# Optimization experiments

Hardware: AMD Instinct MI355X
Metric: run time of the kernel (lower is better)

Reference implementation:

```python
import jax, jax.numpy as jnp
import numpy as np

EPS = 1e-6
NEG = -10000.0

def compute_alibi_slopes(n_head):
    # standard ALiBi slopes for power-of-two head counts: 2^{-8(i+1)/n}
    start = 2.0 ** (-8.0 / n_head)
    return jnp.asarray([start ** (i + 1) for i in range(n_head)], dtype=jnp.float32)

def setup_inputs() -> dict:
    key = jax.random.key(0)
    k1, k2, k3 = jax.random.split(key, 3)
    B, T, C, H = 2, 2048, 1024, 16
    x = jax.random.normal(k1, (B, T, C), dtype=jnp.float32)
    # torch nn.Linear weights are [out_features, in_features]
    w_qkv = jax.random.normal(k2, (3 * C, C), dtype=jnp.float32) * (C ** -0.5)
    w_out = jax.random.normal(k3, (C, C), dtype=jnp.float32) * (C ** -0.5)
    alibi_slopes = compute_alibi_slopes(H)
    return {"x": x, "w_qkv": w_qkv, "w_out": w_out, "alibi_slopes": alibi_slopes}

def rational_softmax(scores, eps=EPS):
    # algebraic sigmoid 0.5*(1 + x/sqrt(1+x^2)) normalized along last axis
    num = 0.5 * (1.0 + scores * jax.lax.rsqrt(1.0 + scores * scores))
    return num / (jnp.sum(num, axis=-1, keepdims=True) + eps)

def reference(x, w_qkv, w_out, alibi_slopes):
    B, T, C = x.shape
    H = alibi_slopes.shape[0]
    D = C // H
    scale = 1.0 / jnp.sqrt(jnp.float32(D))
    qkv = (x @ w_qkv.T).reshape(B, T, 3, H, D)
    qkv = jnp.transpose(qkv, (2, 0, 3, 1, 4))  # [3,B,H,T,D]
    q, k, v = qkv[0], qkv[1], qkv[2]
    scores = jnp.einsum("bhtd,bhsd->bhts", q, k) * scale  # [B,H,T,T]
    pos = jnp.arange(T)
    rel = pos[:, None] - pos[None, :]  # [T,T]
    alibi = -jnp.abs(rel).astype(jnp.float32) * alibi_slopes[None, :, None, None]
    scores = scores + alibi
    causal = rel < 0  # strictly upper triangle (j > i)
    scores = jnp.where(causal[None, None], NEG, scores)
    probs = rational_softmax(scores, EPS)
    out = jnp.einsum("bhts,bhsd->bhtd", probs, v)  # [B,H,T,D]
    out = jnp.transpose(out, (0, 2, 1, 3)).reshape(B, T, C)
    return out @ w_out.T
```

## Files before the change

### kernel.cpp

```cpp
#include <hip/hip_runtime.h>
#include <stdint.h>

typedef __attribute__((ext_vector_type(8))) short bf16x8;
typedef __attribute__((ext_vector_type(4))) float f32x4;
typedef __attribute__((ext_vector_type(16))) float f32x16;

#define MFMA_16x16x32(a, b, c) __builtin_amdgcn_mfma_f32_16x16x32_bf16((a), (b), (c), 0, 0, 0)
#define MFMA_32x32x16(a, b, c) __builtin_amdgcn_mfma_f32_32x32x16_bf16((a), (b), (c), 0, 0, 0)

__device__ __forceinline__ short f2bf(float f) {
  union { float f; uint32_t u; } x;
  x.f = f;
  uint32_t r = x.u + 0x7fffu + ((x.u >> 16) & 1u);
  return (short)(r >> 16);
}

__device__ __forceinline__ uint32_t cvt_pk_bf16(float lo, float hi) {
  uint32_t r;
  asm("v_cvt_pk_bf16_f32 %0, %1, %2" : "=v"(r) : "v"(lo), "v"(hi));
  return r;
}

__device__ __forceinline__ void gload_lds16(const short* g, short* l) {
  __builtin_amdgcn_global_load_lds(
      (const __attribute__((address_space(1))) void*)g,
      (__attribute__((address_space(3))) void*)l, 16, 0, 0);
}

__global__ __launch_bounds__(256) void cast_all(const float* __restrict__ x,
                                                const float* __restrict__ wq,
                                                const float* __restrict__ wo,
                                                short* __restrict__ xb,
                                                short* __restrict__ wqb,
                                                short* __restrict__ wob) {
  int i = blockIdx.x * 256 + threadIdx.x;
  const float* s;
  short* d;
  int off;
  float sc = 1.0f;
  if (i < 524288) { s = x; d = xb; off = i; }
  else if (i < 917504) {
    s = wq; d = wqb; off = i - 524288;
    if (off < 131072) sc = 0.125f;
  }
  else { s = wo; d = wob; off = i - 917504; }
  const float4* sp = (const float4*)s;
  float4 v0 = sp[(size_t)off * 2 + 0];
  float4 v1 = sp[(size_t)off * 2 + 1];
  bf16x8 o;
  o[0] = f2bf(v0.x * sc); o[1] = f2bf(v0.y * sc); o[2] = f2bf(v0.z * sc); o[3] = f2bf(v0.w * sc);
  o[4] = f2bf(v1.x * sc); o[5] = f2bf(v1.y * sc); o[6] = f2bf(v1.z * sc); o[7] = f2bf(v1.w * sc);
  *(bf16x8*)(d + (size_t)off * 8) = o;
}

template <int OUT_BF16>
__global__ __launch_bounds__(512, 2) void gemm256(const short* __restrict__ A,
                                                  const short* __restrict__ B,
                                                  void* __restrict__ Cp,
                                                  int M, int N, int K, int ntN) {
  __shared__ short Al[2][2][128 * 64];
  __shared__ short Bl[2][2][128 * 64];

  const int tid = threadIdx.x;
  const int wv = tid >> 6, lane = tid & 63;
  const int wr = wv >> 2, wc = wv & 3;
  const int lrow = lane & 15, kgrp = lane >> 4;
  const int l3 = lrow & 7;
  const int ck0 = ((kgrp ^ l3)) * 8;
  const int ck1 = ((kgrp ^ l3) ^ 4) * 8;

  const int nwg = gridDim.x;
  const int orig = blockIdx.x;
  const int wg = (orig & 7) * (nwg >> 3) + (orig >> 3);
  const int by = wg / ntN, bx = wg % ntN;
  const int row0 = by * 256, col0 = bx * 256;

  const int r_ = tid >> 3;
  const int cs_ = ((tid & 7) ^ (r_ & 7)) * 8;

  const int NT = K >> 6;
  const int NI = NT >> 1;
  const int NTm1 = NT - 1;

  auto stgA = [&](int slot, int h, int j, int kt) {
    gload_lds16(A + (size_t)(row0 + h * 128 + j * 64 + r_) * K + kt * 64 + cs_,
                &Al[slot][h][j * 4096 + wv * 512]);
  };
  auto stgB = [&](int slot, int h, int j, int kt) {
    gload_lds16(B + (size_t)(col0 + h * 128 + j * 64 + r_) * K + kt * 64 + cs_,
                &Bl[slot][h][j * 4096 + wv * 512]);
  };

  f32x4 acc[8][4] = {};

  const int boff = ((wc & 1) * 64 + lrow) * 64;
  const int bh = wc >> 1;

  stgB(0, 0, 0, 0); stgB(0, 0, 1, 0); stgB(0, 1, 0, 0); stgB(0, 1, 1, 0);
  stgA(0, 0, 0, 0); stgA(0, 0, 1, 0); stgA(0, 1, 0, 0); stgA(0, 1, 1, 0);
  stgB(1, 0, 0, 1); stgB(1, 0, 1, 1); stgB(1, 1, 0, 1); stgB(1, 1, 1, 1);
  asm volatile("s_waitcnt vmcnt(4)" ::: "memory");
  __builtin_amdgcn_s_barrier();

  for (int i = 0; i < NI; ++i) {
    const int ktB1 = (2 * i + 1);
    const int ktP2 = (2 * i + 2 > NTm1) ? NTm1 : 2 * i + 2;
    const int ktP3 = (2 * i + 3 > NTm1) ? NTm1 : 2 * i + 3;
#pragma unroll
    for (int s = 0; s < 2; ++s) {
      bf16x8 bfr[4][2];
#pragma unroll
      for (int q = 0; q < 4; ++q) {
        if (q == 0) {
#pragma unroll
          for (int n = 0; n < 4; ++n) {
            bfr[n][0] = *(const bf16x8*)(&Bl[s][bh][boff + n * 1024 + ck0]);
            bfr[n][1] = *(const bf16x8*)(&Bl[s][bh][boff + n * 1024 + ck1]);
          }
        }
        bf16x8 afr[2][2];
#pragma unroll
        for (int mm = 0; mm < 2; ++mm) {
          const int m = q * 2 + mm;
          afr[mm][0] = *(const bf16x8*)(&Al[s][wr][lrow * 64 + m * 1024 + ck0]);
          afr[mm][1] = *(const bf16x8*)(&Al[s][wr][lrow * 64 + m * 1024 + ck1]);
        }
        if (s == 0) {
          if (q == 0) { stgA(1, 0, 0, ktB1); stgA(1, 0, 1, ktB1); stgA(1, 1, 0, ktB1); stgA(1, 1, 1, ktB1); }
          else if (q == 1) { stgB(0, 0, 0, ktP2); stgB(0, 0, 1, ktP2); }
          else if (q == 2) { stgB(0, 1, 0, ktP2); stgB(0, 1, 1, ktP2); }
        } else {
          if (q == 0) { stgA(0, 0, 0, ktP2); stgA(0, 0, 1, ktP2); stgA(0, 1, 0, ktP2); stgA(0, 1, 1, ktP2); }
          else if (q == 1) { stgB(1, 0, 0, ktP3); stgB(1, 0, 1, ktP3); }
          else if (q == 2) { stgB(1, 1, 0, ktP3); stgB(1, 1, 1, ktP3); }
        }
        __builtin_amdgcn_sched_barrier(0);
        __builtin_amdgcn_s_barrier();
        asm volatile("s_waitcnt lgkmcnt(0)" ::: "memory");
        __builtin_amdgcn_sched_barrier(0);
        __builtin_amdgcn_s_setprio(1);
#pragma unroll
        for (int mm = 0; mm < 2; ++mm)
#pragma unroll
          for (int n = 0; n < 4; ++n)
#pragma unroll
            for (int kk = 0; kk < 2; ++kk)
              acc[q * 2 + mm][n] = MFMA_16x16x32(afr[mm][kk], bfr[n][kk], acc[q * 2 + mm][n]);
        __builtin_amdgcn_s_setprio(0);
        __builtin_amdgcn_sched_barrier(0);
        if (q == 3) {
          asm volatile("s_waitcnt vmcnt(4)" ::: "memory");
        }
        __builtin_amdgcn_s_barrier();
      }
    }
  }

  asm volatile("s_waitcnt vmcnt(0)" ::: "memory");

#pragma unroll
  for (int m = 0; m < 8; ++m) {
    const int grow = row0 + wr * 128 + m * 16 + kgrp * 4;
#pragma unroll
    for (int n = 0; n < 4; ++n) {
      const int gcol = col0 + wc * 64 + n * 16 + lrow;
#pragma unroll
      for (int j = 0; j < 4; ++j) {
        const size_t off = (size_t)(grow + j) * N + gcol;
        if (OUT_BF16) ((short*)Cp)[off] = f2bf(acc[m][n][j]);
        else          ((float*)Cp)[off] = acc[m][n][j];
      }
    }
  }
}

template <int OUT_BF16>
__global__ __launch_bounds__(256, 4) void gemm_bt64(const short* __restrict__ A,
                                                    const short* __restrict__ B,
                                                    void* __restrict__ Cp,
                                                    int M, int N, int K) {
  __shared__ short As[2][64 * 64];
  __shared__ short Bs[2][128 * 64];
  const int tid = threadIdx.x;
  const int wave = tid >> 6, lane = tid & 63;
  const int wr = wave >> 1, wc = wave & 1;
  const int row0 = blockIdx.y * 64, col0 = blockIdx.x * 128;
  const int lrow = lane & 15;
  const int kgrp = lane >> 4;
  const int l3 = lrow & 7;

  const int r_ = tid >> 3;
  const int cs_ = ((tid & 7) ^ (r_ & 7)) * 8;

  const int NT = K >> 6;

  auto STG = [&](int buf, int kt) {
#pragma unroll
    for (int it = 0; it < 2; ++it)
      gload_lds16(A + (size_t)(row0 + it * 32 + r_) * K + kt * 64 + cs_,
                  &As[buf][(it * 256 + wave * 64) * 8]);
#pragma unroll
    for (int it = 0; it < 4; ++it)
      gload_lds16(B + (size_t)(col0 + it * 32 + r_) * K + kt * 64 + cs_,
                  &Bs[buf][(it * 256 + wave * 64) * 8]);
  };

  f32x4 acc[2][4] = {};

  STG(0, 0);

  for (int kt = 0; kt < NT; ++kt) {
    __builtin_amdgcn_s_barrier();
    __builtin_amdgcn_sched_barrier(0);
    const int ktn = (kt + 1 >= NT) ? NT - 1 : kt + 1;
    STG((kt + 1) & 1, ktn);
    asm volatile("s_waitcnt vmcnt(6)" ::: "memory");
    __builtin_amdgcn_sched_barrier(0);
    const short* Ab = As[kt & 1];
    const short* Bb = Bs[kt & 1];
#pragma unroll
    for (int kk = 0; kk < 2; ++kk) {
      const int ck = ((kk * 4 + kgrp) ^ l3) * 8;
      bf16x8 a[2], b[4];
#pragma unroll
      for (int m = 0; m < 2; ++m)
        a[m] = *(const bf16x8*)(Ab + (wr * 32 + m * 16 + lrow) * 64 + ck);
#pragma unroll
      for (int n = 0; n < 4; ++n)
        b[n] = *(const bf16x8*)(Bb + (wc * 64 + n * 16 + lrow) * 64 + ck);
#pragma unroll
      for (int m = 0; m < 2; ++m)
#pragma unroll
        for (int n = 0; n < 4; ++n)
          acc[m][n] = MFMA_16x16x32(a[m], b[n], acc[m][n]);
    }
  }

  asm volatile("s_waitcnt vmcnt(0)" ::: "memory");

#pragma unroll
  for (int m = 0; m < 2; ++m) {
    int rbase = row0 + wr * 32 + m * 16 + kgrp * 4;
#pragma unroll
    for (int n = 0; n < 4; ++n) {
      int col = col0 + wc * 64 + n * 16 + lrow;
#pragma unroll
      for (int j = 0; j < 4; ++j) {
        size_t off = (size_t)(rbase + j) * N + col;
        if (OUT_BF16) ((short*)Cp)[off] = f2bf(acc[m][n][j]);
        else          ((float*)Cp)[off] = acc[m][n][j];
      }
    }
  }
}

__global__ __launch_bounds__(256) void transpose_v(const short* __restrict__ qkv,
                                                   short* __restrict__ vt) {
  const int T = 2048;
  __shared__ short sm[64][72];
  const int bh = blockIdx.y, h = bh & 15, b = bh >> 4;
  const int t0 = blockIdx.x * 64;
  const int tid = threadIdx.x;
#pragma unroll
  for (int p = 0; p < 2; ++p) {
    int idx = p * 256 + tid;
    int tl = idx >> 3, d0 = (idx & 7) * 8;
    bf16x8 v = *(const bf16x8*)(qkv + (b * T + t0 + tl) * 3072 + 2048 + h * 64 + d0);
    *(bf16x8*)(&sm[tl][d0]) = v;
  }
  __syncthreads();
#pragma unroll
  for (int p = 0; p < 2; ++p) {
    int idx = p * 256 + tid;
    int d = idx >> 3, ts0 = (idx & 7) * 8;
    bf16x8 o;
#pragma unroll
    for (int j = 0; j < 8; ++j) o[j] = sm[ts0 + j][d];
    *(bf16x8*)(vt + (bh * 64 + d) * T + t0 + ts0) = o;
  }
}

template <bool DIAG>
__device__ __forceinline__ void attn_sub(
    const short* __restrict__ Kb, const short* __restrict__ Vb,
    const bf16x8 (&qf)[4], const f32x16& crun,
    f32x16& acc0, f32x16& acc1, float (&den4)[4],
    int l31, int hi, int shalf, int mbits) {
  const int krow = l31 >> 1;
  const int kc0 = (l31 & 1) * 8 + hi;
  const int ss = shalf;
  __builtin_amdgcn_s_setprio(1);
  const bf16x8 kf0 = *(const bf16x8*)(Kb + (ss * 16 + krow) * 128 + (kc0 ^ krow) * 8);
  f32x16 s = MFMA_32x32x16(kf0, qf[0], crun);
#pragma unroll
  for (int kkd = 1; kkd < 4; ++kkd) {
    const bf16x8 kf = *(const bf16x8*)(Kb + (ss * 16 + krow) * 128 +
                                       ((kc0 + kkd * 2) ^ krow) * 8);
    s = MFMA_32x32x16(kf, qf[kkd], s);
  }
  __builtin_amdgcn_s_setprio(0);
  float nm[16];
#pragma unroll
  for (int v = 0; v < 16; ++v) {
    float x = s[v];
    if (DIAG) x = ((mbits >> v) & 1) ? -10000.0f : x;
    float t = fmaf(x, x, 1.0f);
    float num = fmaf(x * __builtin_amdgcn_rsqf(t), 0.5f, 0.5f);
    den4[v & 3] += num;
    nm[v] = num;
  }
#pragma unroll
  for (int k1 = 0; k1 < 2; ++k1) {
    union { uint32_t u[4]; bf16x8 v8; } pu;
#pragma unroll
    for (int w01 = 0; w01 < 2; ++w01) {
      uint32_t c0 = cvt_pk_bf16(nm[2 * w01 + 8 * k1], nm[2 * w01 + 8 * k1 + 1]);
      uint32_t c1 = cvt_pk_bf16(nm[2 * w01 + 8 * k1 + 4], nm[2 * w01 + 8 * k1 + 5]);
      asm volatile("v_permlane32_swap_b32 %0, %1" : "+v"(c0), "+v"(c1));
      pu.u[w01] = c0;
      pu.u[w01 + 2] = c1;
    }
    const int vsw = ((((l31 & 1) * 8) + ss * 4 + k1 * 2 + hi) ^ krow) * 8;
    const bf16x8 vf0 = *(const bf16x8*)(Vb + krow * 128 + vsw);
    const bf16x8 vf1 = *(const bf16x8*)(Vb + (16 + krow) * 128 + vsw);
    __builtin_amdgcn_s_setprio(1);
    acc0 = MFMA_32x32x16(pu.v8, vf0, acc0);
    acc1 = MFMA_32x32x16(pu.v8, vf1, acc1);
    __builtin_amdgcn_s_setprio(0);
  }
}

__device__ __constant__ int HPAIR[8][2] = {
  {15, 0}, {14, 1}, {13, 2}, {12, 3}, {11, 4}, {10, 5}, {9, 6}, {8, 7}};

__global__ __launch_bounds__(256, 3) void attn_kernel(const short* __restrict__ qkv,
                                                      const short* __restrict__ vt,
                                                      const float* __restrict__ slopes,
                                                      short* __restrict__ attn_out) {
  const int T = 2048, C = 1024, C3 = 3072;
  __shared__ short Kl[3][4096];
  __shared__ short Vl[3][4096];
  __shared__ float denm[64];

  const int tid = threadIdx.x, wv = tid >> 6, lane = tid & 63;
  const int l31 = lane & 31, hi = lane >> 5;
  const int wg = blockIdx.x;
  const int xcd = wg & 7, j = wg >> 3;
  const int bhsel = j & 3;
  const int qi = 31 - (j >> 2);
  const int h = HPAIR[xcd][bhsel & 1];
  const int b = bhsel >> 1;
  const int bh = b * 16 + h;
  const int qsub = wv >> 1, shalf = wv & 1;
  const float slope = slopes[h];
  const float s64 = slope * 64.0f;

  const int W = (int)(45.0f / (64.0f * slope)) + 2;
  const int kt0 = (qi - W > 0) ? (qi - W) : 0;

  int mbits = 0;
#pragma unroll
  for (int v = 0; v < 16; ++v) {
    int s32 = (v & 3) + 8 * (v >> 2) + 4 * hi;
    if (s32 > l31) mbits |= (1 << v);
  }
  int koff[2], voff[2];
#pragma unroll
  for (int p = 0; p < 2; ++p) {
    int idx = p * 256 + tid;
    int rho = idx >> 4, u = idx & 15, c = u ^ (rho & 15);
    koff[p] = (2 * rho + (c >> 3)) * C3 + (c & 7) * 8;
    voff[p] = (2 * rho + (c >> 3)) * T + (c & 7) * 8;
  }
  const short* kbase = qkv + (size_t)b * T * C3 + C + h * 64;
  const short* vbase = vt + (size_t)bh * 64 * T;

  auto STAGE = [&](int bufi, int kt) {
#pragma unroll
    for (int p = 0; p < 2; ++p)
      gload_lds16(kbase + (size_t)kt * 64 * C3 + koff[p], &Kl[bufi][(p * 256 + wv * 64) * 8]);
#pragma unroll
    for (int p = 0; p < 2; ++p)
      gload_lds16(vbase + kt * 64 + voff[p], &Vl[bufi][(p * 256 + wv * 64) * 8]);
  };

  const int qg = qi * 64 + qsub * 32 + l31;
  bf16x8 qf[4];
#pragma unroll
  for (int ks = 0; ks < 4; ++ks)
    qf[ks] = *(const bf16x8*)(qkv + (size_t)(b * T + qg) * C3 + h * 64 + ks * 16 + hi * 8);
  __builtin_amdgcn_sched_barrier(0);

  STAGE(0, kt0);
  STAGE(1, (kt0 + 1 > qi) ? qi : kt0 + 1);

  f32x16 crun;
#pragma unroll
  for (int v = 0; v < 16; ++v) {
    int s32 = (v & 3) + 8 * (v >> 2) + 4 * hi;
    crun[v] = slope * (float)(s32 - l31 + 32 * (shalf - qsub) + 64 * (kt0 - qi));
  }

  f32x16 acc0 = {}, acc1 = {};
  float den4[4] = {0.f, 0.f, 0.f, 0.f};

  int cA = 0;
  for (int kt = kt0; kt < qi; ++kt) {
    asm volatile("s_waitcnt vmcnt(4)" ::: "memory");
    __builtin_amdgcn_s_barrier();
    __builtin_amdgcn_sched_barrier(0);
    int cS = cA + 2; if (cS >= 3) cS -= 3;
    STAGE(cS, (kt + 2 > qi) ? qi : kt + 2);
    attn_sub<false>(Kl[cA], Vl[cA], qf, crun, acc0, acc1, den4, l31, hi, shalf, mbits);
#pragma unroll
    for (int v = 0; v < 16; ++v) crun[v] += s64;
    cA = (cA == 2) ? 0 : cA + 1;
  }
  asm volatile("s_waitcnt vmcnt(4)" ::: "memory");
  __builtin_amdgcn_s_barrier();
  if (!(qsub == 0 && shalf == 1)) {
    if (qsub == 1 && shalf == 0)
      attn_sub<false>(Kl[cA], Vl[cA], qf, crun, acc0, acc1, den4, l31, hi, shalf, mbits);
    else
      attn_sub<true>(Kl[cA], Vl[cA], qf, crun, acc0, acc1, den4, l31, hi, shalf, mbits);
  }
  __syncthreads();

  int sc = cA + 1; if (sc >= 3) sc -= 3;
  float den = (den4[0] + den4[1]) + (den4[2] + den4[3]);
  den += __shfl_xor(den, 32);

  if (shalf == 1) {
    float* mp = (float*)(qsub == 0 ? &Kl[sc][0] : &Vl[sc][0]);
#pragma unroll
    for (int i = 0; i < 16; ++i) {
      mp[i * 64 + lane] = acc0[i];
      mp[(16 + i) * 64 + lane] = acc1[i];
    }
    if (hi == 0) denm[qsub * 32 + l31] = den;
  }
  __syncthreads();

  if (shalf == 0) {
    const float* mp = (const float*)(qsub == 0 ? &Kl[sc][0] : &Vl[sc][0]);
    den += denm[qsub * 32 + l31];
#pragma unroll
    for (int i = 0; i < 16; ++i) {
      acc0[i] += mp[i * 64 + lane];
      acc1[i] += mp[(16 + i) * 64 + lane];
    }
    short* obase = attn_out + (size_t)(b * T + qi * 64 + qsub * 32) * C + h * 64;
#pragma unroll
    for (int v = 0; v < 16; ++v) {
      int ql = (v & 3) + 8 * (v >> 2) + 4 * hi;
      float dv = __int_as_float(__builtin_amdgcn_ds_bpermute(ql << 2, __float_as_int(den)));
      float r = __builtin_amdgcn_rcpf(dv + 1e-6f);
      obase[(size_t)ql * C + l31] = f2bf(acc0[v] * r);
      obase[(size_t)ql * C + 32 + l31] = f2bf(acc1[v] * r);
    }
  }
}

extern "C" void kernel_launch(void* const* d_in, const int* in_sizes, int n_in,
                              void* d_out, int out_size, void* d_ws, size_t ws_size,
                              hipStream_t stream) {
  const float* x      = (const float*)d_in[0];
  const float* w_qkv  = (const float*)d_in[1];
  const float* w_out  = (const float*)d_in[2];
  const float* slopes = (const float*)d_in[3];

  const int B = 2, T = 2048, C = 1024;
  const int M = B * T;
  const int N1 = 3 * C;

  char* ws = (char*)d_ws;
  short* x_bf    = (short*)(ws);
  short* wqkv_bf = (short*)(ws + 8388608);
  short* wout_bf = (short*)(ws + 14680064);
  short* qkv_bf  = (short*)(ws + 16777216);
  short* vt_bf   = (short*)(ws + 41943040);
  short* ao_bf   = (short*)(ws + 50331648);

  cast_all<<<4096, 256, 0, stream>>>(x, w_qkv, w_out, x_bf, wqkv_bf, wout_bf);

  gemm256<1><<<dim3((M / 256) * (N1 / 256)), 512, 0, stream>>>(x_bf, wqkv_bf, qkv_bf,
                                                               M, N1, C, N1 / 256);

  transpose_v<<<dim3(T / 64, 32), 256, 0, stream>>>(qkv_bf, vt_bf);

  attn_kernel<<<1024, 256, 0, stream>>>(qkv_bf, vt_bf, slopes, ao_bf);

  gemm_bt64<0><<<dim3(C / 128, M / 64), 256, 0, stream>>>(ao_bf, wout_bf, (float*)d_out, M, C, C);
}
```

Before: 102.3 us.

## Widen attention workgroups to 128 query rows sharing staged K/V tiles

The attention kernel now launches 512 workgroups of 512 threads, each covering a 128-row query block with four query groups that share the same triple-buffered K/V tiles in LDS. Each thread issues a single LDS-direct load per tile instead of two, and per-wave causal logic decides whether a tile is a full, diagonal-masked, or skipped block. This halves redundant K/V global loads across query blocks. In exchange, the waves above the diagonal idle on the last tile, the ALiBi window is widened to the larger block, and fewer, larger workgroups may reduce scheduling flexibility and load balance.

```diff
diff --git a/kernel.cpp b/kernel.cpp
--- a/kernel.cpp
+++ b/kernel.cpp
@@ -333,30 +333,33 @@
 __device__ __constant__ int HPAIR[8][2] = {
   {15, 0}, {14, 1}, {13, 2}, {12, 3}, {11, 4}, {10, 5}, {9, 6}, {8, 7}};
 
-__global__ __launch_bounds__(256, 3) void attn_kernel(const short* __restrict__ qkv,
+__global__ __launch_bounds__(512, 4) void attn_kernel(const short* __restrict__ qkv,
                                                       const short* __restrict__ vt,
                                                       const float* __restrict__ slopes,
                                                       short* __restrict__ attn_out) {
   const int T = 2048, C = 1024, C3 = 3072;
   __shared__ short Kl[3][4096];
   __shared__ short Vl[3][4096];
-  __shared__ float denm[64];
+  __shared__ float denm[128];
 
   const int tid = threadIdx.x, wv = tid >> 6, lane = tid & 63;
   const int l31 = lane & 31, hi = lane >> 5;
   const int wg = blockIdx.x;
   const int xcd = wg & 7, j = wg >> 3;
   const int bhsel = j & 3;
-  const int qi = 31 - (j >> 2);
+  const int qibase = 15 - (j >> 2);
   const int h = HPAIR[xcd][bhsel & 1];
   const int b = bhsel >> 1;
   const int bh = b * 16 + h;
-  const int qsub = wv >> 1, shalf = wv & 1;
+  const int g = wv >> 1, shalf = wv & 1;
   const float slope = slopes[h];
   const float s64 = slope * 64.0f;
 
+  const int qr0 = qibase * 128;
+  const int qi_hi = 2 * qibase + 1;
   const int W = (int)(45.0f / (64.0f * slope)) + 2;
-  const int kt0 = (qi - W > 0) ? (qi - W) : 0;
+  int kt0 = 2 * qibase - W; if (kt0 < 0) kt0 = 0;
+  const int myq = 4 * qibase + g;
 
   int mbits = 0;
 #pragma unroll
@@ -364,27 +367,18 @@
     int s32 = (v & 3) + 8 * (v >> 2) + 4 * hi;
     if (s32 > l31) mbits |= (1 << v);
   }
-  int koff[2], voff[2];
-#pragma unroll
-  for (int p = 0; p < 2; ++p) {
-    int idx = p * 256 + tid;
-    int rho = idx >> 4, u = idx & 15, c = u ^ (rho & 15);
-    koff[p] = (2 * rho + (c >> 3)) * C3 + (c & 7) * 8;
-    voff[p] = (2 * rho + (c >> 3)) * T + (c & 7) * 8;
-  }
+  const int rho = tid >> 4, u_ = tid & 15, c_ = u_ ^ (rho & 15);
+  const int koff = (2 * rho + (c_ >> 3)) * C3 + (c_ & 7) * 8;
+  const int voff = (2 * rho + (c_ >> 3)) * T + (c_ & 7) * 8;
   const short* kbase = qkv + (size_t)b * T * C3 + C + h * 64;
   const short* vbase = vt + (size_t)bh * 64 * T;
 
   auto STAGE = [&](int bufi, int kt) {
-#pragma unroll
-    for (int p = 0; p < 2; ++p)
-      gload_lds16(kbase + (size_t)kt * 64 * C3 + koff[p], &Kl[bufi][(p * 256 + wv * 64) * 8]);
-#pragma unroll
-    for (int p = 0; p < 2; ++p)
-      gload_lds16(vbase + kt * 64 + voff[p], &Vl[bufi][(p * 256 + wv * 64) * 8]);
+    gload_lds16(kbase + (size_t)kt * 64 * C3 + koff, &Kl[bufi][wv * 512]);
+    gload_lds16(vbase + kt * 64 + voff, &Vl[bufi][wv * 512]);
   };
 
-  const int qg = qi * 64 + qsub * 32 + l31;
+  const int qg = qr0 + g * 32 + l31;
   bf16x8 qf[4];
 #pragma unroll
   for (int ks = 0; ks < 4; ++ks)
@@ -392,64 +386,58 @@
   __builtin_amdgcn_sched_barrier(0);
 
   STAGE(0, kt0);
-  STAGE(1, (kt0 + 1 > qi) ? qi : kt0 + 1);
+  STAGE(1, (kt0 + 1 > qi_hi) ? qi_hi : kt0 + 1);
 
   f32x16 crun;
 #pragma unroll
   for (int v = 0; v < 16; ++v) {
     int s32 = (v & 3) + 8 * (v >> 2) + 4 * hi;
-    crun[v] = slope * (float)(s32 - l31 + 32 * (shalf - qsub) + 64 * (kt0 - qi));
+    crun[v] = slope * (float)(kt0 * 64 + shalf * 32 + s32 - qg);
   }
 
   f32x16 acc0 = {}, acc1 = {};
   float den4[4] = {0.f, 0.f, 0.f, 0.f};
 
   int cA = 0;
-  for (int kt = kt0; kt < qi; ++kt) {
+  for (int kt = kt0; kt <= qi_hi; ++kt) {
     asm volatile("s_waitcnt vmcnt(4)" ::: "memory");
     __builtin_amdgcn_s_barrier();
     __builtin_amdgcn_sched_barrier(0);
     int cS = cA + 2; if (cS >= 3) cS -= 3;
-    STAGE(cS, (kt + 2 > qi) ? qi : kt + 2);
-    attn_sub<false>(Kl[cA], Vl[cA], qf, crun, acc0, acc1, den4, l31, hi, shalf, mbits);
+    STAGE(cS, (kt + 2 > qi_hi) ? qi_hi : kt + 2);
+    const int drel = (2 * kt + shalf) - myq;
+    if (drel < 0)
+      attn_sub<false>(Kl[cA], Vl[cA], qf, crun, acc0, acc1, den4, l31, hi, shalf, mbits);
+    else if (drel == 0)
+      attn_sub<true>(Kl[cA], Vl[cA], qf, crun, acc0, acc1, den4, l31, hi, shalf, mbits);
 #pragma unroll
     for (int v = 0; v < 16; ++v) crun[v] += s64;
     cA = (cA == 2) ? 0 : cA + 1;
   }
-  asm volatile("s_waitcnt vmcnt(4)" ::: "memory");
-  __builtin_amdgcn_s_barrier();
-  if (!(qsub == 0 && shalf == 1)) {
-    if (qsub == 1 && shalf == 0)
-      attn_sub<false>(Kl[cA], Vl[cA], qf, crun, acc0, acc1, den4, l31, hi, shalf, mbits);
-    else
-      attn_sub<true>(Kl[cA], Vl[cA], qf, crun, acc0, acc1, den4, l31, hi, shalf, mbits);
-  }
   __syncthreads();
 
-  int sc = cA + 1; if (sc >= 3) sc -= 3;
   float den = (den4[0] + den4[1]) + (den4[2] + den4[3]);
   den += __shfl_xor(den, 32);
 
+  float* mp = (g < 3) ? (float*)&Kl[g][0] : (float*)&Vl[0][0];
   if (shalf == 1) {
-    float* mp = (float*)(qsub == 0 ? &Kl[sc][0] : &Vl[sc][0]);
 #pragma unroll
     for (int i = 0; i < 16; ++i) {
       mp[i * 64 + lane] = acc0[i];
       mp[(16 + i) * 64 + lane] = acc1[i];
     }
-    if (hi == 0) denm[qsub * 32 + l31] = den;
+    if (hi == 0) denm[g * 32 + l31] = den;
   }
   __syncthreads();
 
   if (shalf == 0) {
-    const float* mp = (const float*)(qsub == 0 ? &Kl[sc][0] : &Vl[sc][0]);
-    den += denm[qsub * 32 + l31];
+    den += denm[g * 32 + l31];
 #pragma unroll
     for (int i = 0; i < 16; ++i) {
       acc0[i] += mp[i * 64 + lane];
       acc1[i] += mp[(16 + i) * 64 + lane];
     }
-    short* obase = attn_out + (size_t)(b * T + qi * 64 + qsub * 32) * C + h * 64;
+    short* obase = attn_out + (size_t)(b * T + qr0 + g * 32) * C + h * 64;
 #pragma unroll
     for (int v = 0; v < 16; ++v) {
       int ql = (v & 3) + 8 * (v >> 2) + 4 * hi;
@@ -488,7 +476,7 @@
 
   transpose_v<<<dim3(T / 64, 32), 256, 0, stream>>>(qkv_bf, vt_bf);
 
-  attn_kernel<<<1024, 256, 0, stream>>>(qkv_bf, vt_bf, slopes, ao_bf);
+  attn_kernel<<<512, 512, 0, stream>>>(qkv_bf, vt_bf, slopes, ao_bf);
 
   gemm_bt64<0><<<dim3(C / 128, M / 64), 256, 0, stream>>>(ao_bf, wout_bf, (float*)d_out, M, C, C);
 }
```

New measurement: 113.8 us. 1.11x slower.
